# Performance work log

Measured on AMD Instinct MI355X. Metric: run time of the kernel, lower is better.

The kernel has to match this reference:

```python
import jax, jax.numpy as jnp
import numpy as np

SLOPE = 25.0          # fast_sigmoid surrogate slope
H_THRESH = 1.0        # hidden_threshold
O_THRESH = 1.0        # output_threshold
CH_THRESH = 1.0       # cochlea LIF threshold
W_MIN, W_MAX, BITS = 0.001, 1.0, 5

@jax.custom_vjp
def spike(v):
    return (v > 0).astype(v.dtype)

def _spike_fwd(v):
    return spike(v), v

def _spike_bwd(v, g):
    # fast_sigmoid surrogate gradient: 1 / (slope*|v| + 1)^2
    return (g / (SLOPE * jnp.abs(v) + 1.0) ** 2,)

spike.defvjp(_spike_fwd, _spike_bwd)

def fake_quant(w):
    # STE fake quantization (same forward value in train/eval)
    levels = 2 ** BITS
    scale = (W_MAX - W_MIN) / (levels - 1)
    wc = jnp.clip(w, W_MIN, W_MAX)
    q = jnp.round((wc - W_MIN) / scale) * scale + W_MIN
    return wc + jax.lax.stop_gradient(q - wc)

def lif(cur, mem, beta, thresh):
    # snnTorch Leaky, reset_mechanism='subtract': reset from previous mem (detached),
    # then integrate, then fire on new mem.
    reset = jax.lax.stop_gradient(spike(mem - thresh))
    mem = jnp.clip(beta, 0.0, 1.0) * mem + cur - reset * thresh
    spk = spike(mem - thresh)
    return spk, mem

def setup_inputs() -> dict:
    key = jax.random.key(0)
    ks = jax.random.split(key, 8)
    B, T, IN, HID, OUT = 64, 500, 256, 512, 35
    return {
        "x": jax.random.normal(ks[0], (B, T, 1), dtype=jnp.float32),
        "Wch": jax.random.normal(ks[1], (IN, 1), dtype=jnp.float32) * (1.0),
        "W1": jax.random.uniform(ks[2], (HID, IN), minval=W_MIN, maxval=W_MAX, dtype=jnp.float32),
        "W2": jax.random.uniform(ks[3], (HID, HID), minval=W_MIN, maxval=W_MAX, dtype=jnp.float32),
        "W3": jax.random.uniform(ks[4], (HID, HID), minval=W_MIN, maxval=W_MAX, dtype=jnp.float32),
        "W4": jax.random.uniform(ks[5], (OUT, HID), minval=W_MIN, maxval=W_MAX, dtype=jnp.float32),
        "cochlea_betas": jax.random.uniform(ks[6], (IN,), minval=0.05, maxval=0.99, dtype=jnp.float32),
        "beta1": jnp.float32(0.95),
        "beta2": jnp.float32(0.95),
        "beta3": jnp.float32(0.95),
        "beta4": jnp.float32(0.9),
    }

def reference(x, Wch, W1, W2, W3, W4, cochlea_betas, beta1, beta2, beta3, beta4):
    B = x.shape[0]
    # weights are static across time: quantize once, outside the scan
    q1, q2, q3, q4 = fake_quant(W1), fake_quant(W2), fake_quant(W3), fake_quant(W4)
    init = (
        jnp.zeros((B, Wch.shape[0]), x.dtype),  # ch_mem
        jnp.zeros((B, W1.shape[0]), x.dtype),   # mem1
        jnp.zeros((B, W2.shape[0]), x.dtype),   # mem2
        jnp.zeros((B, W3.shape[0]), x.dtype),   # mem3
        jnp.zeros((B, W4.shape[0]), x.dtype),   # mem4
    )

    def step(carry, xt):
        chm, m1, m2, m3, m4 = carry
        ch_spk, chm = lif(xt @ Wch.T, chm, cochlea_betas, CH_THRESH)
        s1, m1 = lif(ch_spk @ q1.T, m1, beta1, H_THRESH)
        s2, m2 = lif(s1 @ q2.T, m2, beta2, H_THRESH)
        s3, m3 = lif(s2 @ q3.T, m3, beta3, H_THRESH)
        s4, m4 = lif(s3 @ q4.T, m4, beta4, O_THRESH)
        return (chm, m1, m2, m3, m4), (s1, s2, s3, s4, m4)

    _, (spk1, spk2, spk3, spk4, mem4) = jax.lax.scan(step, init, jnp.swapaxes(x, 0, 1))
    # each is [T, B, features], matching torch.stack(..., dim=0)
    return spk1, spk2, spk3, spk4, mem4
```

## Files before the change

kernel.cpp:

```cpp
#include <hip/hip_runtime.h>
#include <stdint.h>

#define TT   500
#define BB   64
#define IND  256
#define HD   512
#define OD   35

typedef __attribute__((ext_vector_type(4))) int i32x4;

#define SCALE_F ((float)((1.0 - 0.001) / 31.0))

__device__ __forceinline__ void load16_lds(const int8_t* g, int8_t* l) {
  __builtin_amdgcn_global_load_lds((const __attribute__((address_space(1))) void*)g,
                                   (__attribute__((address_space(3))) void*)l, 16, 0, 0);
}

__global__ __launch_bounds__(256) void k_prep_cochlea(const float* __restrict__ W1,
                                                      const float* __restrict__ W2,
                                                      const float* __restrict__ W3,
                                                      const float* __restrict__ W4,
                                                      int8_t* __restrict__ wk1,
                                                      int8_t* __restrict__ wk2,
                                                      int8_t* __restrict__ wk3,
                                                      int8_t* __restrict__ wk4,
                                                      const float* __restrict__ x,
                                                      const float* __restrict__ Wch,
                                                      const float* __restrict__ cbetas,
                                                      int8_t* __restrict__ chs) {
  __shared__ float xs[TT];
  if (blockIdx.x < 2688) {
    int id = blockIdx.x * 256 + threadIdx.x;
    const float* W; int8_t* wk; int idx, K, H;
    if (id < 131072)       { idx = id;          W = W1; wk = wk1; K = 256; H = 512; }
    else if (id < 393216)  { idx = id - 131072; W = W2; wk = wk2; K = 512; H = 512; }
    else if (id < 655360)  { idx = id - 393216; W = W3; wk = wk3; K = 512; H = 512; }
    else                   { idx = id - 655360; W = W4; wk = wk4; K = 512; H = 35;  }
    int h = idx / K;
    int k = idx - h * K;
    int8_t bits = 0;
    if (h < H) {
      float w  = W[h * K + k];
      float wc = fminf(1.0f, fmaxf(0.001f, w));
      float v  = (wc - 0.001f) / SCALE_F;
      float q  = rintf(v);
      bits = (int8_t)q;
    }
    wk[idx] = bits;
  } else {
    int b = blockIdx.x - 2688;
    int i = threadIdx.x;
    for (int t = threadIdx.x; t < TT; t += 256) xs[t] = x[b * TT + t];
    __syncthreads();
    float w    = Wch[i];
    float beta = fminf(1.0f, fmaxf(0.0f, cbetas[i]));
    float mem  = 0.0f;
    for (int t = 0; t < TT; ++t) {
      float cur = __fmul_rn(xs[t], w);
      int   rs  = (mem > 1.0f);
      float t2  = __fadd_rn(__fmul_rn(beta, mem), cur);
      mem = rs ? __fsub_rn(t2, 1.0f) : t2;
      int spk = (mem > 1.0f);
      chs[(size_t)(t * BB + b) * IND + i] = (int8_t)spk;
    }
  }
}

template<int K, bool LAST>
__global__ __launch_bounds__(256, 2) void k_layer(const int8_t* __restrict__ A,
                                                  const int8_t* __restrict__ Bw,
                                                  const float* __restrict__ pbeta,
                                                  float* __restrict__ spk_out,
                                                  int8_t* __restrict__ s_out,
                                                  float* __restrict__ mem_out) {
  constexpr int CH = K / 16;
  constexpr int KS = K / 64;
  __shared__ __align__(16) int8_t Bs[64 * K];
  __shared__ __align__(16) int8_t As[64 * K];
  __shared__ float curbuf[64][64];
  int tid = threadIdx.x, lane = tid & 63, w = tid >> 6;
  int b, h0;
  if (LAST) { b = blockIdx.x;      h0 = 0; }
  else      { b = blockIdx.x & 63; h0 = (blockIdx.x >> 6) * 64; }
  float beta = fminf(1.0f, fmaxf(0.0f, *pbeta));
#pragma unroll
  for (int i = 0; i < CH / 4; ++i) {
    int L = i * 256 + tid;
    int row = L / CH, sl = L % CH;
    int kg = (sl & ~7) | ((sl & 7) ^ (row & 7));
    load16_lds(Bw + (size_t)(h0 + row) * K + kg * 16, &Bs[(i * 256 + w * 64) * 16]);
  }
#pragma unroll
  for (int i = 0; i < CH / 4; ++i) {
    int L = i * 256 + tid;
    int r = L / CH, sl = L % CH;
    int kg = (sl & ~7) | ((sl & 7) ^ (r & 7));
    load16_lds(A + ((size_t)r * 64 + b) * K + kg * 16, &As[(i * 256 + w * 64) * 16]);
  }
  __syncthreads();
  const double DSCALE = (double)SCALE_F;
  const double DWMIN  = (double)0.001f;
  float mem = 0.0f;
  int lr = lane & 15, lk = lane >> 4;
  int arow = w * 16 + lr;
  i32x4 breg[4][KS];
#pragma unroll
  for (int cg = 0; cg < 4; ++cg)
#pragma unroll
    for (int ks = 0; ks < KS; ++ks) {
      int kc = ks * 4 + lk;
      int s0 = (kc & ~7) | ((kc & 7) ^ (lr & 7));
      breg[cg][ks] = *(const i32x4*)&Bs[(cg * 16 + lr) * K + s0 * 16];
    }
  const i32x4 ones = {0x01010101, 0x01010101, 0x01010101, 0x01010101};
  for (int g = 0; g < 8; ++g) {
    i32x4 acc0 = {0,0,0,0}, acc1 = {0,0,0,0}, acc2 = {0,0,0,0}, acc3 = {0,0,0,0};
    i32x4 acc4 = {0,0,0,0};
#pragma unroll
    for (int ks = 0; ks < KS; ++ks) {
      int kc = ks * 4 + lk;
      int s0 = (kc & ~7) | ((kc & 7) ^ (lr & 7));
      i32x4 av = *(const i32x4*)&As[arow * K + s0 * 16];
      acc0 = __builtin_amdgcn_mfma_i32_16x16x64_i8(av, breg[0][ks], acc0, 0, 0, 0);
      acc1 = __builtin_amdgcn_mfma_i32_16x16x64_i8(av, breg[1][ks], acc1, 0, 0, 0);
      acc2 = __builtin_amdgcn_mfma_i32_16x16x64_i8(av, breg[2][ks], acc2, 0, 0, 0);
      acc3 = __builtin_amdgcn_mfma_i32_16x16x64_i8(av, breg[3][ks], acc3, 0, 0, 0);
      acc4 = __builtin_amdgcn_mfma_i32_16x16x64_i8(av, ones, acc4, 0, 0, 0);
    }
    int pr = w * 16 + lk * 4;
#pragma unroll
    for (int i = 0; i < 4; ++i) {
      double nd = (double)acc4[i] * DWMIN;
      curbuf[pr + i][ 0 + lr] = (float)((double)acc0[i] * DSCALE + nd);
      curbuf[pr + i][16 + lr] = (float)((double)acc1[i] * DSCALE + nd);
      curbuf[pr + i][32 + lr] = (float)((double)acc2[i] * DSCALE + nd);
      curbuf[pr + i][48 + lr] = (float)((double)acc3[i] * DSCALE + nd);
    }
    __syncthreads();
    if (g < 7) {
#pragma unroll
      for (int i = 0; i < CH / 4; ++i) {
        int L = i * 256 + tid;
        int r = L / CH, sl = L % CH;
        int kg = (sl & ~7) | ((sl & 7) ^ (r & 7));
        int t = (g + 1) * 64 + r; if (t > 499) t = 499;
        load16_lds(A + ((size_t)t * 64 + b) * K + kg * 16, &As[(i * 256 + w * 64) * 16]);
      }
    }
    if (w == 0) {
      float curA[16], curB[16];
#define LOADQ(dst, q)                                                         \
      { _Pragma("unroll") for (int r = 0; r < 16; ++r)                        \
          dst[r] = curbuf[(q) * 16 + r][lane]; }
#define CHAINQ(src, q)                                                        \
      { _Pragma("unroll") for (int r = 0; r < 16; ++r) {                      \
          int t = g * 64 + (q) * 16 + r;                                      \
          int   rs = (mem > 1.0f);                                            \
          float t2 = __fadd_rn(__fmul_rn(beta, mem), src[r]);                 \
          mem = rs ? __fsub_rn(t2, 1.0f) : t2;                                \
          int spk = (mem > 1.0f);                                             \
          if (t < 500) {                                                      \
            int row = t * 64 + b;                                             \
            if (!LAST) {                                                      \
              __builtin_nontemporal_store(spk ? 1.0f : 0.0f,                  \
                  &spk_out[(size_t)t * 32768 + (b << 9) + h0 + lane]);        \
              s_out[(size_t)row * 512 + h0 + lane] = (int8_t)spk;             \
            } else if (lane < OD) {                                           \
              __builtin_nontemporal_store(spk ? 1.0f : 0.0f,                  \
                  &spk_out[(size_t)t * (BB * OD) + b * OD + lane]);           \
              __builtin_nontemporal_store(mem,                                \
                  &mem_out[(size_t)t * (BB * OD) + b * OD + lane]);           \
            }                                                                 \
          } } }
      LOADQ(curA, 0)
      LOADQ(curB, 1)
      CHAINQ(curA, 0)
      LOADQ(curA, 2)
      CHAINQ(curB, 1)
      LOADQ(curB, 3)
      CHAINQ(curA, 2)
      CHAINQ(curB, 3)
#undef LOADQ
#undef CHAINQ
    }
    __syncthreads();
  }
}

extern "C" void kernel_launch(void* const* d_in, const int* in_sizes, int n_in,
                              void* d_out, int out_size, void* d_ws, size_t ws_size,
                              hipStream_t stream) {
  const float* x      = (const float*)d_in[0];
  const float* Wch    = (const float*)d_in[1];
  const float* W1     = (const float*)d_in[2];
  const float* W2     = (const float*)d_in[3];
  const float* W3     = (const float*)d_in[4];
  const float* W4     = (const float*)d_in[5];
  const float* cbetas = (const float*)d_in[6];
  const float* b1     = (const float*)d_in[7];
  const float* b2     = (const float*)d_in[8];
  const float* b3     = (const float*)d_in[9];
  const float* b4     = (const float*)d_in[10];

  uint8_t* ws = (uint8_t*)d_ws;
  int8_t*   wk1   = (int8_t*)(ws + 0);
  int8_t*   wk2   = (int8_t*)(ws + 131072);
  int8_t*   wk3   = (int8_t*)(ws + 393216);
  int8_t*   wk4   = (int8_t*)(ws + 655360);
  int8_t*   chs   = (int8_t*)(ws + 688128);
  int8_t*   sbufA = (int8_t*)(ws + 8880128);
  int8_t*   sbufB = (int8_t*)(ws + 25264128);

  float* out  = (float*)d_out;
  float* spk1 = out;
  float* spk2 = out + 16384000;
  float* spk3 = out + 32768000;
  float* spk4 = out + 49152000;
  float* mem4 = out + 50272000;

  k_prep_cochlea<<<2752, 256, 0, stream>>>(W1, W2, W3, W4, wk1, wk2, wk3, wk4,
                                           x, Wch, cbetas, chs);

  k_layer<256, false><<<512, 256, 0, stream>>>(chs,   wk1, b1, spk1, sbufA, nullptr);
  k_layer<512, false><<<512, 256, 0, stream>>>(sbufA, wk2, b2, spk2, sbufB, nullptr);
  k_layer<512, false><<<512, 256, 0, stream>>>(sbufB, wk3, b3, spk3, sbufA, nullptr);
  k_layer<512, true ><<<64,  256, 0, stream>>>(sbufA, wk4, b4, spk4, nullptr, mem4);
}
```

Measured before the change: 343.5 us.

## Offload next-tile A staging to idle waves and relax barrier waits

Waves 1-3 now do the global-to-LDS staging of the next A time tile, while wave 0 runs the serial LIF recurrence. This is meant to overlap the loads with the scalar chain instead of every wave issuing them. The LDS swizzle changes from an XOR pattern to a rotation ((sl - 5*row) mod CH). The two __syncthreads are replaced with explicit waitcnt plus s_barrier, so wave 0 skips waiting on vmcnt. This relies on manual memory ordering: if any wave consumes LDS before its loads land, results can be wrong.

```diff
diff --git a/kernel.cpp b/kernel.cpp
--- a/kernel.cpp
+++ b/kernel.cpp
@@ -66,6 +66,23 @@
   }
 }
 
+template<int K>
+__device__ __forceinline__ void stage_a(const int8_t* __restrict__ A, int8_t* As,
+                                        int b, int gnext, int w, int lane) {
+  constexpr int CH = K / 16;
+  if (w > 0) {
+    constexpr int per = (CH + 2) / 3;
+    int jlo = (w - 1) * per, jhi = jlo + per; if (jhi > CH) jhi = CH;
+    for (int j = jlo; j < jhi; ++j) {
+      int L = j * 64 + lane;
+      int r = L / CH, sl = L % CH;
+      int kg = (sl - 5 * r) & (CH - 1);
+      int t = gnext * 64 + r; if (t > 499) t = 499;
+      load16_lds(A + ((size_t)t * 64 + b) * K + kg * 16, &As[j * 1024]);
+    }
+  }
+}
+
 template<int K, bool LAST>
 __global__ __launch_bounds__(256, 2) void k_layer(const int8_t* __restrict__ A,
                                                   const int8_t* __restrict__ Bw,
@@ -87,16 +104,10 @@
   for (int i = 0; i < CH / 4; ++i) {
     int L = i * 256 + tid;
     int row = L / CH, sl = L % CH;
-    int kg = (sl & ~7) | ((sl & 7) ^ (row & 7));
+    int kg = (sl - 5 * row) & (CH - 1);
     load16_lds(Bw + (size_t)(h0 + row) * K + kg * 16, &Bs[(i * 256 + w * 64) * 16]);
   }
-#pragma unroll
-  for (int i = 0; i < CH / 4; ++i) {
-    int L = i * 256 + tid;
-    int r = L / CH, sl = L % CH;
-    int kg = (sl & ~7) | ((sl & 7) ^ (r & 7));
-    load16_lds(A + ((size_t)r * 64 + b) * K + kg * 16, &As[(i * 256 + w * 64) * 16]);
-  }
+  stage_a<K>(A, As, b, 0, w, lane);
   __syncthreads();
   const double DSCALE = (double)SCALE_F;
   const double DWMIN  = (double)0.001f;
@@ -108,9 +119,9 @@
   for (int cg = 0; cg < 4; ++cg)
 #pragma unroll
     for (int ks = 0; ks < KS; ++ks) {
-      int kc = ks * 4 + lk;
-      int s0 = (kc & ~7) | ((kc & 7) ^ (lr & 7));
-      breg[cg][ks] = *(const i32x4*)&Bs[(cg * 16 + lr) * K + s0 * 16];
+      int row = cg * 16 + lr;
+      int s0 = (ks * 4 + lk + 5 * row) & (CH - 1);
+      breg[cg][ks] = *(const i32x4*)&Bs[row * K + s0 * 16];
     }
   const i32x4 ones = {0x01010101, 0x01010101, 0x01010101, 0x01010101};
   for (int g = 0; g < 8; ++g) {
@@ -118,8 +129,7 @@
     i32x4 acc4 = {0,0,0,0};
 #pragma unroll
     for (int ks = 0; ks < KS; ++ks) {
-      int kc = ks * 4 + lk;
-      int s0 = (kc & ~7) | ((kc & 7) ^ (lr & 7));
+      int s0 = (ks * 4 + lk + 5 * arow) & (CH - 1);
       i32x4 av = *(const i32x4*)&As[arow * K + s0 * 16];
       acc0 = __builtin_amdgcn_mfma_i32_16x16x64_i8(av, breg[0][ks], acc0, 0, 0, 0);
       acc1 = __builtin_amdgcn_mfma_i32_16x16x64_i8(av, breg[1][ks], acc1, 0, 0, 0);
@@ -136,17 +146,11 @@
       curbuf[pr + i][32 + lr] = (float)((double)acc2[i] * DSCALE + nd);
       curbuf[pr + i][48 + lr] = (float)((double)acc3[i] * DSCALE + nd);
     }
-    __syncthreads();
-    if (g < 7) {
-#pragma unroll
-      for (int i = 0; i < CH / 4; ++i) {
-        int L = i * 256 + tid;
-        int r = L / CH, sl = L % CH;
-        int kg = (sl & ~7) | ((sl & 7) ^ (r & 7));
-        int t = (g + 1) * 64 + r; if (t > 499) t = 499;
-        load16_lds(A + ((size_t)t * 64 + b) * K + kg * 16, &As[(i * 256 + w * 64) * 16]);
-      }
-    }
+    __builtin_amdgcn_sched_barrier(0);
+    asm volatile("s_waitcnt lgkmcnt(0)" ::: "memory");
+    __builtin_amdgcn_s_barrier();
+    __builtin_amdgcn_sched_barrier(0);
+    if (g < 7) stage_a<K>(A, As, b, g + 1, w, lane);
     if (w == 0) {
       float curA[16], curB[16];
 #define LOADQ(dst, q)                                                         \
@@ -183,7 +187,11 @@
 #undef LOADQ
 #undef CHAINQ
     }
-    __syncthreads();
+    __builtin_amdgcn_sched_barrier(0);
+    if (w == 0) asm volatile("s_waitcnt lgkmcnt(0)" ::: "memory");
+    else        asm volatile("s_waitcnt vmcnt(0) lgkmcnt(0)" ::: "memory");
+    __builtin_amdgcn_s_barrier();
+    __builtin_amdgcn_sched_barrier(0);
   }
 }
 
```

New measurement: 339.3 us, median of 2. No clear change (-1.2%).
